# Performance work log

Measured on AMD Instinct MI355X. Metric: run time of the kernel, lower is better.

Reference implementation:

```python
import jax, jax.numpy as jnp
import numpy as np

B, C, T, H0, W0 = 4, 512, 4, 63, 63
NUM_IMAGES = 4
CP = C // (NUM_IMAGES * 3)   # 42, compare-branch channels
CC = C // 2                  # 256, attention channels
AGG_IN = C + CP * 3 * NUM_IMAGES  # 1016


def setup_inputs() -> dict:
    key = jax.random.key(0)
    ks = jax.random.split(key, 9)
    w = lambda k, shape: jax.random.normal(k, shape, jnp.float32) * 0.05
    return {
        "x": jax.random.normal(ks[0], (B, C, T, H0, W0), jnp.float32),
        "Wq": w(ks[1], (CC, C)),
        "Wm": w(ks[2], (CC, C)),
        "Wv": w(ks[3], (CC, C)),
        "Wcat": w(ks[4], (CP, C)),
        "Wsub": w(ks[5], (CP, CC)),
        "Wmul": w(ks[6], (CP, CC)),
        "g_cat": jnp.ones((CP,), jnp.float32), "b_cat": jnp.zeros((CP,), jnp.float32),
        "g_sub": jnp.ones((CP,), jnp.float32), "b_sub": jnp.zeros((CP,), jnp.float32),
        "g_mul": jnp.ones((CP,), jnp.float32), "b_mul": jnp.zeros((CP,), jnp.float32),
        "Wagg": w(ks[7], (C, AGG_IN)),
        "g_agg": jnp.ones((C,), jnp.float32), "b_agg": jnp.zeros((C,), jnp.float32),
    }


def _bn(y, g, b):
    # training-mode batch norm over all dims except channel (dim 1)
    m = jnp.mean(y, axis=(0, 2, 3, 4), keepdims=True)
    v = jnp.var(y, axis=(0, 2, 3, 4), keepdims=True)
    return (y - m) * jax.lax.rsqrt(v + 1e-5) * g.reshape(1, -1, 1, 1, 1) + b.reshape(1, -1, 1, 1, 1)


def _forward(x, Wq, Wm, Wv, Wcat, Wsub, Wmul, g_cat, b_cat, g_sub, b_sub,
             g_mul, b_mul, Wagg, g_agg, b_agg):
    # max_pool3d kernel (1,3,3) stride (1,2,2)
    xp = jax.lax.reduce_window(x, -jnp.inf, jax.lax.max,
                               (1, 1, 1, 3, 3), (1, 1, 1, 2, 2), 'VALID')
    Bn, Cn, Tn, Hn, Wn = xp.shape
    cc, hw, thw = Cn // 2, Hn * Wn, Tn * Hn * Wn

    # --- Attend ---
    Q = jnp.einsum('oc,bcthw->bothw', Wq, xp)
    M = jnp.einsum('oc,bcthw->bothw', Wm, xp)
    V = jnp.einsum('oc,bcthw->bothw', Wv, xp)
    scores = jnp.einsum('bcq,bck->bqk', Q.reshape(Bn, cc, thw),
                        M.reshape(Bn, cc, thw)) / np.sqrt(cc).astype(np.float32)
    # softmax over memory pixels within each memory frame
    A = jax.nn.softmax(scores.reshape(Bn, thw, Tn, hw), axis=-1)  # (B, q=t*h*w, Tm, HWm)
    Vf = V.reshape(Bn, cc, Tn, hw).transpose(0, 2, 3, 1)          # (B, Tm, HWm, cc)
    R = jnp.einsum('bqmj,bmjc->bmqc', A, Vf)                      # (B, Tm, THWq, cc)
    R = R.reshape(Bn, Tn, Tn, Hn, Wn, cc).transpose(0, 5, 1, 2, 3, 4)  # (B, cc, Tm, Tq, H, W)

    # --- Compare ---
    Rflat = R.reshape(Bn, cc, Tn * Tn, Hn, Wn)
    Vexp = jnp.broadcast_to(V[:, :, :, None], (Bn, cc, Tn, Tn, Hn, Wn)).reshape(
        Bn, cc, Tn * Tn, Hn, Wn)
    conv = lambda Wk, y: jnp.einsum('oc,bcshw->boshw', Wk, y)
    Ccat = _bn(conv(Wcat, jnp.concatenate([Rflat, Vexp], axis=1)), g_cat, b_cat)
    Csub = _bn(conv(Wsub, Rflat - Vexp), g_sub, b_sub)
    Cmul = _bn(conv(Wmul, Rflat * Vexp), g_mul, b_mul)
    Cfeat = jax.nn.relu(jnp.concatenate([Ccat, Csub, Cmul], axis=1)
                        .reshape(Bn, -1, Tn, Hn, Wn))

    # --- Aggregate ---
    Y = jnp.concatenate([R.mean(axis=3), V, Cfeat], axis=1)  # (B, 1016, T, H, W)
    Z = _bn(jnp.einsum('oc,bcthw->bothw', Wagg, Y), g_agg, b_agg)
    return jax.nn.relu(xp + Z)


def reference(x, Wq, Wm, Wv, Wcat, Wsub, Wmul, g_cat, b_cat, g_sub, b_sub,
              g_mul, b_mul, Wagg, g_agg, b_agg):
    return _forward(x, Wq, Wm, Wv, Wcat, Wsub, Wmul, g_cat, b_cat, g_sub,
                    b_sub, g_mul, b_mul, Wagg, g_agg, b_agg)
```

## Files before the change

### kernel.cpp

```cpp
#include <hip/hip_runtime.h>
#include <math.h>

constexpr int Bb   = 4;
constexpr int Cch  = 512;
constexpr int HW   = 961;
constexpr int THW  = 3844;
constexpr int NCMP = 126;
constexpr int NPIX = Bb * Cch * THW;
constexpr int Hp = 31, Wp = 31, H0c = 63, W0c = 63;
constexpr int VP = 1024;
#define BN_EPS 1e-5f

typedef __attribute__((ext_vector_type(4))) float floatx4;
typedef __attribute__((ext_vector_type(8))) __bf16 bf16x8;
typedef __attribute__((ext_vector_type(8))) unsigned short ushort8;
typedef __attribute__((ext_vector_type(4))) unsigned short ushort4v;

static __device__ __forceinline__ unsigned short f2bf(float x) {
    unsigned int u = __builtin_bit_cast(unsigned int, x);
    u += 0x7fff + ((u >> 16) & 1);
    return (unsigned short)(u >> 16);
}
static __device__ __forceinline__ float bf2f(unsigned short u) {
    return __builtin_bit_cast(float, ((unsigned int)u) << 16);
}

static __device__ __forceinline__ void gl_lds16(const unsigned short* g,
                                                unsigned short* l) {
    __builtin_amdgcn_global_load_lds(
        (const __attribute__((address_space(1))) void*)g,
        (__attribute__((address_space(3))) void*)l, 16, 0, 0);
}

__global__ __launch_bounds__(256) void k_prep_w(
    const float* __restrict__ Wcat, const float* __restrict__ Wsub,
    const float* __restrict__ Wmul, const float* __restrict__ Wagg,
    unsigned short* __restrict__ Wpk, unsigned short* __restrict__ Wab,
    unsigned short* __restrict__ Vbf) {
    int idx = blockIdx.x * 256 + threadIdx.x;
    if (idx < 24576) {
        int row = idx >> 9, k = idx & 511;
        Wpk[idx] = (row < 42) ? f2bf(Wcat[row * 512 + k]) : 0;
    } else if (idx < 36864) {
        int i = idx - 24576;
        int row = i >> 8, k = i & 255;
        Wpk[idx] = (row < 42) ? f2bf(Wsub[row * 256 + k]) : 0;
    } else if (idx < 49152) {
        int i = idx - 36864;
        int row = i >> 8, k = i & 255;
        Wpk[idx] = (row < 42) ? f2bf(Wmul[row * 256 + k]) : 0;
    } else if (idx < 49152 + 524288) {
        int i = idx - 49152;
        int row = i >> 10, k = i & 1023;
        Wab[i] = (k < 1016) ? f2bf(Wagg[(size_t)row * 1016 + k]) : 0;
    } else if (idx < 573440 + 258048) {
        int i = idx - 573440;
        int row = i / 63, k = i - row * 63;
        Vbf[(size_t)row * VP + 961 + k] = 0;
    }
}

__global__ __launch_bounds__(256) void k_pool(const float* __restrict__ x,
                                              float* __restrict__ xp) {
    int idx = blockIdx.x * 256 + threadIdx.x;
    if (idx >= NPIX) return;
    int w = idx % Wp;
    int h = (idx / Wp) % Hp;
    int bct = idx / HW;
    const float* src = x + (size_t)bct * (H0c * W0c) + (2 * h) * W0c + 2 * w;
    float m = -INFINITY;
    #pragma unroll
    for (int i = 0; i < 3; ++i) {
        m = fmaxf(m, src[i * W0c + 0]);
        m = fmaxf(m, src[i * W0c + 1]);
        m = fmaxf(m, src[i * W0c + 2]);
    }
    xp[idx] = m;
}

__global__ __launch_bounds__(256) void k_xpose(const float* __restrict__ xp,
                                               unsigned short* __restrict__ Xh,
                                               unsigned short* __restrict__ Xl) {
    __shared__ float T[64][65];
    const int p0 = blockIdx.x * 64;
    const int c0 = blockIdx.y * 64;
    const int b  = blockIdx.z;
    const int tid = threadIdx.x;
    {
        int px4 = (tid & 15) * 4;
        int cb = tid >> 4;
        #pragma unroll
        for (int i = 0; i < 4; ++i) {
            int c = cb + i * 16;
            int p = p0 + px4;
            const float* src = xp + ((size_t)(b * Cch + c0 + c)) * THW + p;
            float4 v;
            if (p + 3 < THW) {
                v = *(const float4*)src;
            } else {
                v.x = (p     < THW) ? src[0] : 0.f;
                v.y = (p + 1 < THW) ? src[1] : 0.f;
                v.z = (p + 2 < THW) ? src[2] : 0.f;
                v.w = (p + 3 < THW) ? src[3] : 0.f;
            }
            T[c][px4] = v.x; T[c][px4 + 1] = v.y;
            T[c][px4 + 2] = v.z; T[c][px4 + 3] = v.w;
        }
    }
    __syncthreads();
    {
        int px = tid >> 2;
        int cs = (tid & 3) * 16;
        int p = p0 + px;
        if (p < THW) {
            ushort8 hi[2], lo[2];
            #pragma unroll
            for (int j = 0; j < 16; ++j) {
                float v = T[cs + j][px];
                unsigned short h = f2bf(v);
                hi[j >> 3][j & 7] = h;
                lo[j >> 3][j & 7] = f2bf(v - bf2f(h));
            }
            size_t base = ((size_t)b * THW + p) * 512 + c0 + cs;
            *(ushort8*)&Xh[base]     = hi[0];
            *(ushort8*)&Xh[base + 8] = hi[1];
            *(ushort8*)&Xl[base]     = lo[0];
            *(ushort8*)&Xl[base + 8] = lo[1];
        }
    }
}

__global__ __launch_bounds__(256) void k_qmv_mfma(
    const unsigned short* __restrict__ Xh, const unsigned short* __restrict__ Xl,
    const float* __restrict__ Wq, const float* __restrict__ Wm,
    const float* __restrict__ Wv,
    unsigned short* __restrict__ Qbf, unsigned short* __restrict__ Mbf,
    float* __restrict__ Vcl, unsigned short* __restrict__ Vbf) {
    __shared__ unsigned short Whs[128 * 64] __attribute__((aligned(16)));
    __shared__ unsigned short Wls[128 * 64] __attribute__((aligned(16)));
    const int p0  = blockIdx.x * 128;
    const int sel = blockIdx.y >> 1;
    const int ocr = (blockIdx.y & 1) * 128;
    const int b   = blockIdx.z;
    const float* Wbase = ((sel == 0) ? Wq : (sel == 1) ? Wm : Wv) + (size_t)ocr * 512;
    const int tid = threadIdx.x;
    const int wv = tid >> 6, lane = tid & 63;
    const int l15 = lane & 15, quad = lane >> 4;

    floatx4 acc[8][2];
    #pragma unroll
    for (int i = 0; i < 8; ++i)
        #pragma unroll
        for (int h = 0; h < 2; ++h) acc[i][h] = (floatx4){0.f, 0.f, 0.f, 0.f};

    for (int kc = 0; kc < 512; kc += 64) {
        __syncthreads();
        #pragma unroll
        for (int i = 0; i < 4; ++i) {
            int t = i * 256 + tid;
            int row = t >> 3, c8 = t & 7;
            const float* wr = Wbase + (size_t)row * 512 + kc + c8 * 8;
            float v[8];
            *(float4*)&v[0] = *(const float4*)wr;
            *(float4*)&v[4] = *(const float4*)(wr + 4);
            ushort8 hi, lo;
            #pragma unroll
            for (int j = 0; j < 8; ++j) {
                unsigned short h = f2bf(v[j]);
                hi[j] = h;
                lo[j] = f2bf(v[j] - bf2f(h));
            }
            int addr = row * 64 + ((c8 ^ (row & 7)) << 3);
            *(ushort8*)&Whs[addr] = hi;
            *(ushort8*)&Wls[addr] = lo;
        }
        __syncthreads();
        #pragma unroll
        for (int half = 0; half < 2; ++half) {
            int px = p0 + (wv * 2 + half) * 16 + l15;
            int pxc = min(px, THW - 1);
            const unsigned short* xh = Xh + ((size_t)b * THW + pxc) * 512 + kc;
            const unsigned short* xl = Xl + ((size_t)b * THW + pxc) * 512 + kc;
            #pragma unroll
            for (int ks = 0; ks < 2; ++ks) {
                ushort8 bh = *(const ushort8*)&xh[ks * 32 + quad * 8];
                ushort8 bl = *(const ushort8*)&xl[ks * 32 + quad * 8];
                #pragma unroll
                for (int oct = 0; oct < 8; ++oct) {
                    int row = oct * 16 + l15;
                    int ca = row * 64 + (((ks * 4 + quad) ^ (row & 7)) << 3);
                    ushort8 ah = *(const ushort8*)&Whs[ca];
                    ushort8 al = *(const ushort8*)&Wls[ca];
                    acc[oct][half] = __builtin_amdgcn_mfma_f32_16x16x32_bf16(
                        __builtin_bit_cast(bf16x8, ah),
                        __builtin_bit_cast(bf16x8, bh), acc[oct][half], 0, 0, 0);
                    acc[oct][half] = __builtin_amdgcn_mfma_f32_16x16x32_bf16(
                        __builtin_bit_cast(bf16x8, ah),
                        __builtin_bit_cast(bf16x8, bl), acc[oct][half], 0, 0, 0);
                    acc[oct][half] = __builtin_amdgcn_mfma_f32_16x16x32_bf16(
                        __builtin_bit_cast(bf16x8, al),
                        __builtin_bit_cast(bf16x8, bh), acc[oct][half], 0, 0, 0);
                }
            }
        }
    }
    if (sel < 2) {
        unsigned short* outbf = sel ? Mbf : Qbf;
        const float scale = sel ? 1.0f : 0.0625f;
        #pragma unroll
        for (int half = 0; half < 2; ++half) {
            int px = p0 + (wv * 2 + half) * 16 + l15;
            if (px < THW) {
                #pragma unroll
                for (int oct = 0; oct < 8; ++oct) {
                    int ch = ocr + oct * 16 + quad * 4;
                    ushort4v v;
                    #pragma unroll
                    for (int r = 0; r < 4; ++r) v[r] = f2bf(acc[oct][half][r] * scale);
                    *(ushort4v*)&outbf[((size_t)b * THW + px) * 256 + ch] = v;
                }
            }
        }
    } else {
        #pragma unroll
        for (int half = 0; half < 2; ++half) {
            int px = p0 + (wv * 2 + half) * 16 + l15;
            if (px < THW) {
                int m = px / HW;
                int key = px - m * HW;
                size_t vbbase = (size_t)(b * 4 + m) * 256;
                #pragma unroll
                for (int oct = 0; oct < 8; ++oct) {
                    int ch = ocr + oct * 16 + quad * 4;
                    float4 fv = make_float4(acc[oct][half][0], acc[oct][half][1],
                                            acc[oct][half][2], acc[oct][half][3]);
                    *(float4*)&Vcl[((size_t)b * THW + px) * 256 + ch] = fv;
                    #pragma unroll
                    for (int r = 0; r < 4; ++r)
                        Vbf[(vbbase + ch + r) * VP + key] = f2bf(acc[oct][half][r]);
                }
            }
        }
    }
}

__global__ __launch_bounds__(256, 2) void k_attn_mfma(
    const unsigned short* __restrict__ Qbf, const unsigned short* __restrict__ Mbf,
    const unsigned short* __restrict__ Vbf, unsigned short* __restrict__ Rbf) {
    __shared__ unsigned short Mb[2][16384] __attribute__((aligned(16)));
    __shared__ unsigned short Ps[4096] __attribute__((aligned(16)));
    __shared__ float alpha_s[64];
    __shared__ float l_s[64];

    const int bm = blockIdx.x;
    const int b = bm >> 2, m = bm & 3;
    const int q0 = blockIdx.y * 64;
    const int tid = threadIdx.x;
    const int wv = tid >> 6, lane = tid & 63;
    const int l15 = lane & 15, quad = lane >> 4;
    const int x7 = l15 & 7;

    const size_t mbase = ((size_t)b * THW + m * HW) * 256;
    const size_t vb = (size_t)bm * 256 * VP;

    const int qg = min(q0 + wv * 16 + l15, THW - 1);
    const unsigned short* qp = Qbf + ((size_t)b * THW + qg) * 256 + quad * 8;
    ushort8 qreg[8];
    #pragma unroll
    for (int kci = 0; kci < 8; ++kci)
        qreg[kci] = *(const ushort8*)&qp[kci * 32];

    #pragma unroll
    for (int i = 0; i < 8; ++i) {
        int blk = wv * 8 + i;
        int key = blk * 2 + (lane >> 5);
        int cS = (lane & 31) ^ (key & 7);
        gl_lds16(Mbf + mbase + (size_t)key * 256 + (cS << 3), &Mb[0][blk * 512]);
    }

    floatx4 o[4][4];
    #pragma unroll
    for (int mt = 0; mt < 4; ++mt)
        #pragma unroll
        for (int nt = 0; nt < 4; ++nt) o[mt][nt] = (floatx4){0.f, 0.f, 0.f, 0.f};
    float m_run = -1e30f, l_run = 0.f;

    __syncthreads();

    int cur = 0;
    for (int kt = 0; kt < 16; ++kt) {
        const int k0 = kt * 64;
        const int nv = min(64, HW - k0);
        if (kt < 15) {
            int k0n = k0 + 64;
            #pragma unroll
            for (int i = 0; i < 8; ++i) {
                int blk = wv * 8 + i;
                int key = blk * 2 + (lane >> 5);
                int cS = (lane & 31) ^ (key & 7);
                int kg = min(k0n + key, HW - 1);
                gl_lds16(Mbf + mbase + (size_t)kg * 256 + (cS << 3),
                         &Mb[cur ^ 1][blk * 512]);
            }
        }
        floatx4 sc[4];
        #pragma unroll
        for (int kb = 0; kb < 4; ++kb) sc[kb] = (floatx4){0.f, 0.f, 0.f, 0.f};
        #pragma unroll
        for (int kb = 0; kb < 4; ++kb) {
            const int key = kb * 16 + l15;
            #pragma unroll
            for (int kci = 0; kci < 8; ++kci) {
                ushort8 mf = *(const ushort8*)&Mb[cur][key * 256 +
                    ((((kci << 2) + quad) ^ x7) << 3)];
                sc[kb] = __builtin_amdgcn_mfma_f32_16x16x32_bf16(
                    __builtin_bit_cast(bf16x8, mf),
                    __builtin_bit_cast(bf16x8, qreg[kci]), sc[kb], 0, 0, 0);
            }
        }
        #pragma unroll
        for (int kb = 0; kb < 4; ++kb) {
            #pragma unroll
            for (int r = 0; r < 4; ++r)
                if (kb * 16 + quad * 4 + r >= nv) sc[kb][r] = -1e30f;
        }
        float mx = -1e30f;
        #pragma unroll
        for (int kb = 0; kb < 4; ++kb)
            mx = fmaxf(mx, fmaxf(fmaxf(sc[kb][0], sc[kb][1]),
                                 fmaxf(sc[kb][2], sc[kb][3])));
        mx = fmaxf(mx, __shfl_xor(mx, 16));
        mx = fmaxf(mx, __shfl_xor(mx, 32));
        float m_new = fmaxf(m_run, mx);
        float al = __expf(m_run - m_new);
        float sm = 0.f;
        #pragma unroll
        for (int kb = 0; kb < 4; ++kb) {
            #pragma unroll
            for (int r = 0; r < 4; ++r) {
                float p = __expf(sc[kb][r] - m_new);
                sc[kb][r] = p;
                sm += p;
            }
        }
        sm += __shfl_xor(sm, 16);
        sm += __shfl_xor(sm, 32);
        l_run = l_run * al + sm;
        m_run = m_new;
        if (quad == 0) alpha_s[wv * 16 + l15] = al;
        {
            const int prow = wv * 16 + l15;
            #pragma unroll
            for (int kb = 0; kb < 4; ++kb) {
                ushort4v pk;
                #pragma unroll
                for (int r = 0; r < 4; ++r) pk[r] = f2bf(sc[kb][r]);
                int cW = ((kb << 1) + (quad >> 1)) ^ x7;
                *(ushort4v*)&Ps[prow * 64 + (cW << 3) + ((quad & 1) << 2)] = pk;
            }
        }
        __syncthreads();
        ushort8 bvr[8];
        #pragma unroll
        for (int ks = 0; ks < 2; ++ks)
            #pragma unroll
            for (int nt = 0; nt < 4; ++nt) {
                int ch = wv * 64 + nt * 16 + l15;
                bvr[ks * 4 + nt] = *(const ushort8*)&Vbf[
                    vb + (size_t)ch * VP + k0 + ((((ks << 2) + quad)) << 3)];
            }
        #pragma unroll
        for (int mt = 0; mt < 4; ++mt) {
            float alq[4];
            #pragma unroll
            for (int r = 0; r < 4; ++r) alq[r] = alpha_s[mt * 16 + quad * 4 + r];
            #pragma unroll
            for (int nt = 0; nt < 4; ++nt)
                #pragma unroll
                for (int r = 0; r < 4; ++r) o[mt][nt][r] *= alq[r];
        }
        #pragma unroll
        for (int ks = 0; ks < 2; ++ks) {
            ushort8 af[4];
            #pragma unroll
            for (int mt = 0; mt < 4; ++mt)
                af[mt] = *(const ushort8*)&Ps[(mt * 16 + l15) * 64 +
                    ((((ks << 2) + quad) ^ x7) << 3)];
            #pragma unroll
            for (int nt = 0; nt < 4; ++nt) {
                #pragma unroll
                for (int mt = 0; mt < 4; ++mt)
                    o[mt][nt] = __builtin_amdgcn_mfma_f32_16x16x32_bf16(
                        __builtin_bit_cast(bf16x8, af[mt]),
                        __builtin_bit_cast(bf16x8, bvr[ks * 4 + nt]), o[mt][nt],
                        0, 0, 0);
            }
        }
        __syncthreads();
        cur ^= 1;
    }
    if (quad == 0) l_s[wv * 16 + l15] = l_run;
    __syncthreads();
    #pragma unroll
    for (int mt = 0; mt < 4; ++mt) {
        float invl[4];
        #pragma unroll
        for (int r = 0; r < 4; ++r) invl[r] = 1.f / l_s[mt * 16 + quad * 4 + r];
        #pragma unroll
        for (int nt = 0; nt < 4; ++nt) {
            int ch = wv * 64 + nt * 16 + l15;
            #pragma unroll
            for (int r = 0; r < 4; ++r) {
                int qrow = mt * 16 + quad * 4 + r;
                Mb[0][qrow * 256 + ch] = f2bf(o[mt][nt][r] * invl[r]);
            }
        }
    }
    __syncthreads();
    #pragma unroll
    for (int k = 0; k < 8; ++k) {
        int idx = k * 256 + tid;
        int qrow = idx >> 5, c = idx & 31;
        int q = q0 + qrow;
        if (q < THW) {
            ushort8 v = *(const ushort8*)&Mb[0][qrow * 256 + c * 8];
            __builtin_nontemporal_store(v,
                (ushort8*)&Rbf[((size_t)bm * THW + q) * 256 + c * 8]);
        }
    }
}

__global__ __launch_bounds__(256) void k_cmp(
    const unsigned short* __restrict__ Rbf, const float* __restrict__ Vcl,
    const unsigned short* __restrict__ Wpk, float* __restrict__ Pc) {
    __shared__ unsigned short Ws[24576] __attribute__((aligned(16)));
    const int strip = blockIdx.x;
    const int s = blockIdx.y;
    const int b = blockIdx.z >> 1, kind = blockIdx.z & 1;
    const int m = s >> 2, tq = s & 3;
    const int tid = threadIdx.x;
    const int wv = tid >> 6, lane = tid & 63;
    const int l15 = lane & 15, quad = lane >> 4;

    const unsigned short* wsrc = Wpk + (kind ? 24576 : 0);
    for (int i = tid; i < 3072; i += 256) {
        int row, ch, stride_us;
        if (kind == 0) { row = i >> 6; ch = i & 63; stride_us = 512; }
        else           { row = i >> 5; ch = i & 31; stride_us = 256; }
        ushort8 v = *(const ushort8*)&wsrc[i * 8];
        *(ushort8*)&Ws[row * stride_us + ((ch ^ (row & 7)) << 3)] = v;
    }
    __syncthreads();

    const size_t rbase = ((size_t)(b * 4 + m) * THW + tq * HW) * 256;
    const size_t vbase = ((size_t)b * THW + m * HW) * 256;

    #pragma unroll
    for (int half = 0; half < 2; ++half) {
        int pxt = wv * 2 + half;
        int hw = strip * 128 + pxt * 16 + l15;
        int hwc = min(hw, HW - 1);
        const unsigned short* rrow = Rbf + rbase + (size_t)hwc * 256;
        const float* vrow = Vcl + vbase + (size_t)hwc * 256;
        bf16x8 fr[8], fs[8];
        #pragma unroll
        for (int ks = 0; ks < 8; ++ks) {
            ushort8 r8 = *(const ushort8*)&rrow[ks * 32 + quad * 8];
            float vv[8];
            *(float4*)&vv[0] = *(const float4*)&vrow[ks * 32 + quad * 8];
            *(float4*)&vv[4] = *(const float4*)&vrow[ks * 32 + quad * 8 + 4];
            bf16x8 a, c;
            if (kind == 0) {
                a = __builtin_bit_cast(bf16x8, r8);
                #pragma unroll
                for (int j = 0; j < 8; ++j) c[j] = (__bf16)vv[j];
            } else {
                #pragma unroll
                for (int j = 0; j < 8; ++j) {
                    float rj = bf2f(r8[j]);
                    a[j] = (__bf16)(rj - vv[j]);
                    c[j] = (__bf16)(rj * vv[j]);
                }
            }
            fr[ks] = a; fs[ks] = c;
        }
        floatx4 acc[6];
        #pragma unroll
        for (int i = 0; i < 6; ++i) acc[i] = (floatx4){0.f, 0.f, 0.f, 0.f};
        if (kind == 0) {
            #pragma unroll
            for (int ks = 0; ks < 16; ++ks) {
                bf16x8 bfr = (ks < 8) ? fr[ks] : fs[ks - 8];
                #pragma unroll
                for (int cit = 0; cit < 3; ++cit) {
                    int row = cit * 16 + l15;
                    ushort8 aw = *(const ushort8*)&Ws[row * 512 + (((ks * 4 + quad) ^ (row & 7)) << 3)];
                    acc[cit] = __builtin_amdgcn_mfma_f32_16x16x32_bf16(
                        __builtin_bit_cast(bf16x8, aw), bfr, acc[cit], 0, 0, 0);
                }
            }
        } else {
            #pragma unroll
            for (int ks = 0; ks < 8; ++ks) {
                #pragma unroll
                for (int cit = 0; cit < 6; ++cit) {
                    int row = cit * 16 + l15;
                    ushort8 aw = *(const ushort8*)&Ws[row * 256 + (((ks * 4 + quad) ^ (row & 7)) << 3)];
                    bf16x8 bfr = (cit < 3) ? fr[ks] : fs[ks];
                    acc[cit] = __builtin_amdgcn_mfma_f32_16x16x32_bf16(
                        __builtin_bit_cast(bf16x8, aw), bfr, acc[cit], 0, 0, 0);
                }
            }
        }
        if (hw < HW) {
            if (kind == 0) {
                #pragma unroll
                for (int cit = 0; cit < 3; ++cit)
                    #pragma unroll
                    for (int r = 0; r < 4; ++r) {
                        int ci = cit * 16 + quad * 4 + r;
                        if (ci < 42)
                            Pc[((size_t)(b * NCMP + ci) * 16 + s) * HW + hw] = acc[cit][r];
                    }
            } else {
                #pragma unroll
                for (int cit = 0; cit < 6; ++cit)
                    #pragma unroll
                    for (int r = 0; r < 4; ++r) {
                        int cl = (cit % 3) * 16 + quad * 4 + r;
                        if (cl < 42) {
                            int ci = (cit < 3 ? 42 : 84) + cl;
                            Pc[((size_t)(b * NCMP + ci) * 16 + s) * HW + hw] = acc[cit][r];
                        }
                    }
            }
        }
    }
}

__global__ __launch_bounds__(256) void k_stats_cmp(
    const float* __restrict__ Pc, const float* __restrict__ g_cat,
    const float* __restrict__ b_cat, const float* __restrict__ g_sub,
    const float* __restrict__ b_sub, const float* __restrict__ g_mul,
    const float* __restrict__ b_mul, float* __restrict__ bnc) {
    const int c = blockIdx.x, tid = threadIdx.x;
    float s = 0.f, q = 0.f;
    for (int i = tid; i < 4 * 16 * HW; i += 256) {
        int bb = i / (16 * HW), r = i - bb * (16 * HW);
        float v = Pc[(size_t)(bb * NCMP + c) * (16 * HW) + r];
        s += v; q += v * v;
    }
    __shared__ float rs[256], rq[256];
    rs[tid] = s; rq[tid] = q;
    __syncthreads();
    for (int off = 128; off > 0; off >>= 1) {
        if (tid < off) { rs[tid] += rs[tid + off]; rq[tid] += rq[tid + off]; }
        __syncthreads();
    }
    if (tid == 0) {
        const float n = 4.f * 16.f * HW;
        float mean = rs[0] / n;
        float var = rq[0] / n - mean * mean;
        float g, bt;
        if (c < 42)       { g = g_cat[c];      bt = b_cat[c]; }
        else if (c < 84)  { g = g_sub[c - 42]; bt = b_sub[c - 42]; }
        else              { g = g_mul[c - 84]; bt = b_mul[c - 84]; }
        float sc = g * rsqrtf(var + BN_EPS);
        bnc[c] = sc;
        bnc[NCMP + c] = bt - mean * sc;
    }
}

__global__ __launch_bounds__(256) void k_build_y(
    const unsigned short* __restrict__ Rbf, const float* __restrict__ Vcl,
    const float* __restrict__ Pc, const float* __restrict__ bnc,
    unsigned short* __restrict__ Ybf) {
    const int strip = blockIdx.x, t = blockIdx.y, b = blockIdx.z;
    const int tid = threadIdx.x;
    const int chl = tid & 31;
    const int hwl = tid >> 5;
    for (int pass = 0; pass < 8; ++pass) {
        int hw = strip * 64 + pass * 8 + hwl;
        if (hw >= HW) continue;
        size_t ybase = ((size_t)b * THW + t * HW + hw) * 1024;
        for (int cb = 0; cb < 8; ++cb) {
            int ch = cb * 128 + chl * 4;
            float v[4];
            if (ch < 256) {
                v[0] = v[1] = v[2] = v[3] = 0.f;
                #pragma unroll
                for (int tq = 0; tq < 4; ++tq) {
                    ushort4v rv = *(const ushort4v*)&Rbf[
                        (((size_t)(b * 4 + t)) * THW + tq * HW + hw) * 256 + ch];
                    v[0] += bf2f(rv[0]); v[1] += bf2f(rv[1]);
                    v[2] += bf2f(rv[2]); v[3] += bf2f(rv[3]);
                }
                v[0] *= 0.25f; v[1] *= 0.25f; v[2] *= 0.25f; v[3] *= 0.25f;
            } else if (ch < 512) {
                float4 vv = *(const float4*)&Vcl[((size_t)b * THW + t * HW + hw) * 256 + (ch - 256)];
                v[0] = vv.x; v[1] = vv.y; v[2] = vv.z; v[3] = vv.w;
            } else if (ch < 1016) {
                int ci = (ch - 512) >> 2;
                float sc = bnc[ci], sh = bnc[NCMP + ci];
                #pragma unroll
                for (int mm = 0; mm < 4; ++mm) {
                    float pv = Pc[(((size_t)(b * NCMP + ci)) * 16 + mm * 4 + t) * HW + hw];
                    v[mm] = fmaxf(fmaf(pv, sc, sh), 0.f);
                }
            } else {
                v[0] = v[1] = v[2] = v[3] = 0.f;
            }
            ushort4v ov;
            #pragma unroll
            for (int i = 0; i < 4; ++i) ov[i] = f2bf(v[i]);
            *(ushort4v*)&Ybf[ybase + ch] = ov;
        }
    }
}

__global__ __launch_bounds__(256) void k_aggm(
    const unsigned short* __restrict__ Wab, const unsigned short* __restrict__ Ybf,
    float* __restrict__ Z) {
    __shared__ unsigned short Wt[16384] __attribute__((aligned(16)));
    const int p0 = blockIdx.x * 128;
    const int oc0 = blockIdx.y * 128;
    const int b = blockIdx.z;
    const int tid = threadIdx.x;
    const int wv = tid >> 6, lane = tid & 63;
    const int l15 = lane & 15, quad = lane >> 4;
    floatx4 acc[8][2];
    #pragma unroll
    for (int i = 0; i < 8; ++i)
        #pragma unroll
        for (int h = 0; h < 2; ++h) acc[i][h] = (floatx4){0.f, 0.f, 0.f, 0.f};
    for (int kc = 0; kc < 8; ++kc) {
        __syncthreads();
        for (int i = tid; i < 2048; i += 256) {
            int row = i >> 4, ch = i & 15;
            ushort8 v = *(const ushort8*)&Wab[(size_t)(oc0 + row) * 1024 + kc * 128 + ch * 8];
            *(ushort8*)&Wt[row * 128 + ((ch ^ (row & 7)) << 3)] = v;
        }
        __syncthreads();
        #pragma unroll
        for (int half = 0; half < 2; ++half) {
            int px = p0 + (wv * 2 + half) * 16 + l15;
            int pxc = min(px, THW - 1);
            const unsigned short* yrow = Ybf + ((size_t)b * THW + pxc) * 1024 + kc * 128;
            #pragma unroll
            for (int ks = 0; ks < 4; ++ks) {
                ushort8 bf = *(const ushort8*)&yrow[ks * 32 + quad * 8];
                #pragma unroll
                for (int oct = 0; oct < 8; ++oct) {
                    int row = oct * 16 + l15;
                    ushort8 af = *(const ushort8*)&Wt[row * 128 + ((((ks * 4 + quad) ^ (row & 7))) << 3)];
                    acc[oct][half] = __builtin_amdgcn_mfma_f32_16x16x32_bf16(
                        __builtin_bit_cast(bf16x8, af),
                        __builtin_bit_cast(bf16x8, bf), acc[oct][half], 0, 0, 0);
                }
            }
        }
    }
    #pragma unroll
    for (int half = 0; half < 2; ++half) {
        int px = p0 + (wv * 2 + half) * 16 + l15;
        if (px < THW) {
            #pragma unroll
            for (int oct = 0; oct < 8; ++oct) {
                int oc = oc0 + oct * 16 + quad * 4;
                #pragma unroll
                for (int r = 0; r < 4; ++r)
                    Z[((size_t)(b * Cch + oc + r)) * THW + px] = acc[oct][half][r];
            }
        }
    }
}

__global__ __launch_bounds__(256) void k_stats_agg(
    const float* __restrict__ Z, const float* __restrict__ g_agg,
    const float* __restrict__ b_agg, float* __restrict__ bna) {
    const int c = blockIdx.x, tid = threadIdx.x;
    float s = 0.f, q = 0.f;
    for (int i = tid; i < 4 * THW; i += 256) {
        int bb = i / THW, p = i - bb * THW;
        float v = Z[((size_t)bb * Cch + c) * THW + p];
        s += v; q += v * v;
    }
    __shared__ float rs[256], rq[256];
    rs[tid] = s; rq[tid] = q;
    __syncthreads();
    for (int off = 128; off > 0; off >>= 1) {
        if (tid < off) { rs[tid] += rs[tid + off]; rq[tid] += rq[tid + off]; }
        __syncthreads();
    }
    if (tid == 0) {
        const float n = 4.f * THW;
        float mean = rs[0] / n;
        float var = rq[0] / n - mean * mean;
        float sc = g_agg[c] * rsqrtf(var + BN_EPS);
        bna[c] = sc;
        bna[Cch + c] = b_agg[c] - mean * sc;
    }
}

__global__ __launch_bounds__(256) void k_final(const float* __restrict__ xp,
                                               const float* __restrict__ Z,
                                               const float* __restrict__ bna,
                                               float* __restrict__ out) {
    int idx = blockIdx.x * 256 + threadIdx.x;
    if (idx >= NPIX) return;
    int c = (idx / THW) & 511;
    out[idx] = fmaxf(fmaf(Z[idx], bna[c], bna[Cch + c]) + xp[idx], 0.f);
}

extern "C" void kernel_launch(void* const* d_in, const int* in_sizes, int n_in,
                              void* d_out, int out_size, void* d_ws, size_t ws_size,
                              hipStream_t stream) {
    const float* x     = (const float*)d_in[0];
    const float* Wq    = (const float*)d_in[1];
    const float* Wm    = (const float*)d_in[2];
    const float* Wv    = (const float*)d_in[3];
    const float* Wcat  = (const float*)d_in[4];
    const float* Wsub  = (const float*)d_in[5];
    const float* Wmul  = (const float*)d_in[6];
    const float* g_cat = (const float*)d_in[7];
    const float* b_cat = (const float*)d_in[8];
    const float* g_sub = (const float*)d_in[9];
    const float* b_sub = (const float*)d_in[10];
    const float* g_mul = (const float*)d_in[11];
    const float* b_mul = (const float*)d_in[12];
    const float* Wagg  = (const float*)d_in[13];
    const float* g_agg = (const float*)d_in[14];
    const float* b_agg = (const float*)d_in[15];
    float* out = (float*)d_out;
    float* ws  = (float*)d_ws;

    float* xp  = ws;
    float* Vcl = xp + 7872512;
    float* bnc = Vcl + 3936256;
    float* bna = bnc + 512;
    unsigned short* Wpk = (unsigned short*)(bna + 1024);
    unsigned short* Wab = Wpk + 49152;
    float* bfreg = (float*)(Wab + 524288);
    unsigned short* Qbf = (unsigned short*)bfreg;
    unsigned short* Mbf = Qbf + 3936256;
    unsigned short* Vbf = Mbf + 3936256;
    unsigned short* Ybf = (unsigned short*)bfreg;
    unsigned short* Rbf = (unsigned short*)(bfreg + 7872512);
    float* Pc = (float*)(Rbf + 15745024);
    float* Z  = (float*)Rbf;
    unsigned short* Xh = Rbf;
    unsigned short* Xl = Xh + 7872512;

    k_prep_w<<<dim3(3248), dim3(256), 0, stream>>>(Wcat, Wsub, Wmul, Wagg, Wpk, Wab, Vbf);
    k_pool<<<dim3((NPIX + 255) / 256), dim3(256), 0, stream>>>(x, xp);
    k_xpose<<<dim3(61, 8, Bb), dim3(256), 0, stream>>>(xp, Xh, Xl);
    k_qmv_mfma<<<dim3(31, 6, Bb), dim3(256), 0, stream>>>(Xh, Xl, Wq, Wm, Wv,
                                                          Qbf, Mbf, Vcl, Vbf);
    k_attn_mfma<<<dim3(16, 61), dim3(256), 0, stream>>>(Qbf, Mbf, Vbf, Rbf);
    k_cmp<<<dim3(8, 16, 8), dim3(256), 0, stream>>>(Rbf, Vcl, Wpk, Pc);
    k_stats_cmp<<<dim3(NCMP), dim3(256), 0, stream>>>(Pc, g_cat, b_cat, g_sub, b_sub,
                                                      g_mul, b_mul, bnc);
    k_build_y<<<dim3(16, 4, Bb), dim3(256), 0, stream>>>(Rbf, Vcl, Pc, bnc, Ybf);
    k_aggm<<<dim3(31, 4, Bb), dim3(256), 0, stream>>>(Wab, Ybf, Z);
    k_stats_agg<<<dim3(Cch), dim3(256), 0, stream>>>(Z, g_agg, b_agg, bna);
    k_final<<<dim3((NPIX + 255) / 256), dim3(256), 0, stream>>>(xp, Z, bna, out);
}
```

Before: 639.0 us.

## Pre-split QMV weights into swizzled bf16 tiles and prefetch V earlier in attention

The Wq/Wm/Wv hi/lo bf16 split and swizzle now happen once in the prep kernel, into a scratch buffer that aliases Pc. The QMV GEMM then loads those weight tiles straight into LDS with global_load_lds instead of converting fp32 weights in every block. The attention kernel issues the V fragment loads before the score computation so their latency overlaps the softmax. It also skips rescaling the output accumulator when every alpha in the wavefront equals one, at the cost of a wave-wide vote.

After: 623.4 us. 2.4% less time.

```diff
diff --git a/kernel.cpp b/kernel.cpp
--- a/kernel.cpp
+++ b/kernel.cpp
@@ -33,10 +33,13 @@
 }
 
 __global__ __launch_bounds__(256) void k_prep_w(
+    const float* __restrict__ Wq, const float* __restrict__ Wm,
+    const float* __restrict__ Wv,
     const float* __restrict__ Wcat, const float* __restrict__ Wsub,
     const float* __restrict__ Wmul, const float* __restrict__ Wagg,
     unsigned short* __restrict__ Wpk, unsigned short* __restrict__ Wab,
-    unsigned short* __restrict__ Vbf) {
+    unsigned short* __restrict__ Vbf,
+    unsigned short* __restrict__ Wh, unsigned short* __restrict__ Wl) {
     int idx = blockIdx.x * 256 + threadIdx.x;
     if (idx < 24576) {
         int row = idx >> 9, k = idx & 511;
@@ -57,6 +60,24 @@
         int i = idx - 573440;
         int row = i / 63, k = i - row * 63;
         Vbf[(size_t)row * VP + 961 + k] = 0;
+    } else if (idx < 831488 + 393216) {
+        int i = idx - 831488;
+        int sel  = i >> 17;
+        int r1   = i & 131071;
+        int ocrb = r1 >> 16;
+        int r2   = r1 & 65535;
+        int kcI  = r2 >> 13;
+        int r3   = r2 & 8191;
+        int row  = r3 >> 6;
+        int c8   = (r3 >> 3) & 7;
+        int j    = r3 & 7;
+        const float* Wsrc = (sel == 0) ? Wq : (sel == 1) ? Wm : Wv;
+        float w = Wsrc[(size_t)(ocrb * 128 + row) * 512 + kcI * 64 + c8 * 8 + j];
+        unsigned short h = f2bf(w);
+        int dst = ((sel * 2 + ocrb) * 8 + kcI) * 8192 + row * 64 +
+                  ((c8 ^ (row & 7)) << 3) + j;
+        Wh[dst] = h;
+        Wl[dst] = f2bf(w - bf2f(h));
     }
 }
 
@@ -132,20 +153,20 @@
 
 __global__ __launch_bounds__(256) void k_qmv_mfma(
     const unsigned short* __restrict__ Xh, const unsigned short* __restrict__ Xl,
-    const float* __restrict__ Wq, const float* __restrict__ Wm,
-    const float* __restrict__ Wv,
+    const unsigned short* __restrict__ Wh, const unsigned short* __restrict__ Wl,
     unsigned short* __restrict__ Qbf, unsigned short* __restrict__ Mbf,
     float* __restrict__ Vcl, unsigned short* __restrict__ Vbf) {
     __shared__ unsigned short Whs[128 * 64] __attribute__((aligned(16)));
     __shared__ unsigned short Wls[128 * 64] __attribute__((aligned(16)));
     const int p0  = blockIdx.x * 128;
     const int sel = blockIdx.y >> 1;
-    const int ocr = (blockIdx.y & 1) * 128;
+    const int ocrb = blockIdx.y & 1;
+    const int ocr = ocrb * 128;
     const int b   = blockIdx.z;
-    const float* Wbase = ((sel == 0) ? Wq : (sel == 1) ? Wm : Wv) + (size_t)ocr * 512;
     const int tid = threadIdx.x;
     const int wv = tid >> 6, lane = tid & 63;
     const int l15 = lane & 15, quad = lane >> 4;
+    const int tbase = ((sel * 2 + ocrb) * 8) * 8192;
 
     floatx4 acc[8][2];
     #pragma unroll
@@ -153,26 +174,15 @@
         #pragma unroll
         for (int h = 0; h < 2; ++h) acc[i][h] = (floatx4){0.f, 0.f, 0.f, 0.f};
 
-    for (int kc = 0; kc < 512; kc += 64) {
+    for (int kcI = 0; kcI < 8; ++kcI) {
+        const int kc = kcI * 64;
         __syncthreads();
+        const int toff = tbase + kcI * 8192;
         #pragma unroll
         for (int i = 0; i < 4; ++i) {
-            int t = i * 256 + tid;
-            int row = t >> 3, c8 = t & 7;
-            const float* wr = Wbase + (size_t)row * 512 + kc + c8 * 8;
-            float v[8];
-            *(float4*)&v[0] = *(const float4*)wr;
-            *(float4*)&v[4] = *(const float4*)(wr + 4);
-            ushort8 hi, lo;
-            #pragma unroll
-            for (int j = 0; j < 8; ++j) {
-                unsigned short h = f2bf(v[j]);
-                hi[j] = h;
-                lo[j] = f2bf(v[j] - bf2f(h));
-            }
-            int addr = row * 64 + ((c8 ^ (row & 7)) << 3);
-            *(ushort8*)&Whs[addr] = hi;
-            *(ushort8*)&Wls[addr] = lo;
+            int blk = wv * 4 + i;
+            gl_lds16(Wh + toff + blk * 512 + lane * 8, &Whs[blk * 512]);
+            gl_lds16(Wl + toff + blk * 512 + lane * 8, &Wls[blk * 512]);
         }
         __syncthreads();
         #pragma unroll
@@ -303,6 +313,15 @@
                          &Mb[cur ^ 1][blk * 512]);
             }
         }
+        ushort8 bvr[8];
+        #pragma unroll
+        for (int ks = 0; ks < 2; ++ks)
+            #pragma unroll
+            for (int nt = 0; nt < 4; ++nt) {
+                int ch = wv * 64 + nt * 16 + l15;
+                bvr[ks * 4 + nt] = *(const ushort8*)&Vbf[
+                    vb + (size_t)ch * VP + k0 + ((((ks << 2) + quad)) << 3)];
+            }
         floatx4 sc[4];
         #pragma unroll
         for (int kb = 0; kb < 4; ++kb) sc[kb] = (floatx4){0.f, 0.f, 0.f, 0.f};
@@ -360,24 +379,18 @@
             }
         }
         __syncthreads();
-        ushort8 bvr[8];
-        #pragma unroll
-        for (int ks = 0; ks < 2; ++ks)
-            #pragma unroll
-            for (int nt = 0; nt < 4; ++nt) {
-                int ch = wv * 64 + nt * 16 + l15;
-                bvr[ks * 4 + nt] = *(const ushort8*)&Vbf[
-                    vb + (size_t)ch * VP + k0 + ((((ks << 2) + quad)) << 3)];
-            }
         #pragma unroll
         for (int mt = 0; mt < 4; ++mt) {
             float alq[4];
             #pragma unroll
             for (int r = 0; r < 4; ++r) alq[r] = alpha_s[mt * 16 + quad * 4 + r];
-            #pragma unroll
-            for (int nt = 0; nt < 4; ++nt)
-                #pragma unroll
-                for (int r = 0; r < 4; ++r) o[mt][nt][r] *= alq[r];
+            if (!__all((alq[0] == 1.f) && (alq[1] == 1.f) &&
+                       (alq[2] == 1.f) && (alq[3] == 1.f))) {
+                #pragma unroll
+                for (int nt = 0; nt < 4; ++nt)
+                    #pragma unroll
+                    for (int r = 0; r < 4; ++r) o[mt][nt][r] *= alq[r];
+            }
         }
         #pragma unroll
         for (int ks = 0; ks < 2; ++ks) {
@@ -750,11 +763,14 @@
     float* Z  = (float*)Rbf;
     unsigned short* Xh = Rbf;
     unsigned short* Xl = Xh + 7872512;
-
-    k_prep_w<<<dim3(3248), dim3(256), 0, stream>>>(Wcat, Wsub, Wmul, Wagg, Wpk, Wab, Vbf);
+    unsigned short* Wh = (unsigned short*)Pc;
+    unsigned short* Wl = Wh + 393216;
+
+    k_prep_w<<<dim3(4784), dim3(256), 0, stream>>>(Wq, Wm, Wv, Wcat, Wsub, Wmul,
+                                                   Wagg, Wpk, Wab, Vbf, Wh, Wl);
     k_pool<<<dim3((NPIX + 255) / 256), dim3(256), 0, stream>>>(x, xp);
     k_xpose<<<dim3(61, 8, Bb), dim3(256), 0, stream>>>(xp, Xh, Xl);
-    k_qmv_mfma<<<dim3(31, 6, Bb), dim3(256), 0, stream>>>(Xh, Xl, Wq, Wm, Wv,
+    k_qmv_mfma<<<dim3(31, 6, Bb), dim3(256), 0, stream>>>(Xh, Xl, Wh, Wl,
                                                           Qbf, Mbf, Vcl, Vbf);
     k_attn_mfma<<<dim3(16, 61), dim3(256), 0, stream>>>(Qbf, Mbf, Vbf, Rbf);
     k_cmp<<<dim3(8, 16, 8), dim3(256), 0, stream>>>(Rbf, Vcl, Wpk, Pc);
```
